# Kernel optimization log

Hardware: AMD Instinct MI355X
Metric: run time of the kernel (lower is better)

## Reference

```python
import jax, jax.numpy as jnp
import numpy as np

B, T, D = 2, 1024, 2048      # batch, seq_len, hidden_size
H, DK = 8, 128               # num_heads, head_k_dim
DV = 2 * DK                  # head_v_dim = head_dim * expand_v
KD, VD = H * DK, H * DV      # key_dim, value_dim
KCONV = 4                    # short conv kernel size
EPS = 1e-5


def _short_conv(x, w):
    # depthwise causal conv1d + SiLU; x: [B,T,C], w: [C,K]
    Klen = w.shape[1]
    xp = jnp.pad(x, ((0, 0), (Klen - 1, 0), (0, 0)))
    win = jnp.stack([xp[:, j:j + x.shape[1], :] for j in range(Klen)], axis=-1)  # [B,T,C,K]
    return jax.nn.silu(jnp.einsum('btck,ck->btc', win, w))


def _l2norm(x):
    return x * jax.lax.rsqrt(jnp.sum(x * x, -1, keepdims=True) + 1e-6)


def reference(hidden_states, q_w, k_w, v_w, a_w, b_w, g_w, o_w,
              q_conv_w, k_conv_w, v_conv_w, A_log, dt_bias, o_norm_w):
    h = hidden_states
    # projections + short depthwise causal conv + SiLU
    q = _short_conv(h @ q_w.T, q_conv_w)        # [B,T,KD]
    k = _short_conv(h @ k_w.T, k_conv_w)        # [B,T,KD]
    v = _short_conv(h @ v_w.T, v_conv_w)        # [B,T,VD]
    q = _l2norm(q.reshape(B, T, H, DK))
    k = _l2norm(k.reshape(B, T, H, DK))
    v = v.reshape(B, T, H, DV)
    beta = jax.nn.sigmoid(h @ b_w.T)                                 # [B,T,H]
    g = -jnp.exp(A_log) * jax.nn.softplus(h @ a_w.T + dt_bias)       # [B,T,H] decay log-gate
    scale = DK ** -0.5

    def step(S, xs):
        # S: [B,H,DK,DV] recurrent state; gated delta rule update
        qt, kt, vt, gt, bt = xs
        S = S * jnp.exp(gt)[..., None, None]
        kv = jnp.einsum('bhk,bhkv->bhv', kt, S)
        u = (vt - kv) * bt[..., None]
        S = S + jnp.einsum('bhk,bhv->bhkv', kt, u)
        ot = jnp.einsum('bhk,bhkv->bhv', qt, S) * scale
        return S, ot

    xs = (q.transpose(1, 0, 2, 3), k.transpose(1, 0, 2, 3), v.transpose(1, 0, 2, 3),
          g.transpose(1, 0, 2), beta.transpose(1, 0, 2))
    S0 = jnp.zeros((B, H, DK, DV), q.dtype)
    _, o = jax.lax.scan(step, S0, xs)
    o = o.transpose(1, 0, 2, 3)                       # [B,T,H,DV]
    # gated RMSNorm (FusedRMSNormGated) + output projection
    gate = (h @ g_w.T).reshape(B, T, H, DV)
    o = o * jax.lax.rsqrt(jnp.mean(o * o, -1, keepdims=True) + EPS) * o_norm_w
    o = o * jax.nn.silu(gate)
    return o.reshape(B, T, VD) @ o_w.T


def setup_inputs() -> dict:
    key = jax.random.key(0)
    ks = jax.random.split(key, 14)
    n = lambda i, shp, sc: jax.random.normal(ks[i], shp, jnp.float32) * sc
    return {
        'hidden_states': n(0, (B, T, D), 1.0),
        'q_w': n(1, (KD, D), 0.02), 'k_w': n(2, (KD, D), 0.02), 'v_w': n(3, (VD, D), 0.02),
        'a_w': n(4, (H, D), 0.02), 'b_w': n(5, (H, D), 0.02),
        'g_w': n(6, (VD, D), 0.02), 'o_w': n(7, (D, VD), 0.02),
        'q_conv_w': n(8, (KD, KCONV), 0.3), 'k_conv_w': n(9, (KD, KCONV), 0.3),
        'v_conv_w': n(10, (VD, KCONV), 0.3),
        'A_log': jnp.log(jax.random.uniform(ks[11], (H,), jnp.float32, 0.5, 16.0)),
        'dt_bias': n(12, (H,), 1.0),
        'o_norm_w': jnp.ones((DV,), jnp.float32),
    }
```

## Files before the change

kernel.cpp:

```cpp
#include <hip/hip_runtime.h>
#include <cstdint>

#define T_LEN 1024
#define NBIG  6400
#define SCALE_Q 0.08838834764831843f

typedef __bf16 bf16;
typedef __bf16 bf16x8 __attribute__((ext_vector_type(8)));
typedef float  f32x4  __attribute__((ext_vector_type(4)));

__device__ __forceinline__ unsigned short f2bf(float f) {
  unsigned int u = __builtin_bit_cast(unsigned int, f);
  u += 0x7FFFu + ((u >> 16) & 1u);
  return (unsigned short)(u >> 16);
}
__device__ __forceinline__ float bf2f(unsigned short u) {
  return __builtin_bit_cast(float, (unsigned int)u << 16);
}
__device__ __forceinline__ float silu_f(float x) { return x / (1.f + __expf(-x)); }

#define GLDS(src, dst) \
  __builtin_amdgcn_global_load_lds( \
      (__attribute__((address_space(1))) void*)(void*)(src), \
      (__attribute__((address_space(3))) void*)(void*)(dst), 16, 0, 0)

__global__ __launch_bounds__(256) void prep_all(
    const float* __restrict__ h,
    const float* __restrict__ qw, const float* __restrict__ kw,
    const float* __restrict__ vw, const float* __restrict__ gw,
    const float* __restrict__ aw, const float* __restrict__ bw,
    unsigned short* __restrict__ hbf, unsigned short* __restrict__ Wb) {
  const int blk = blockIdx.x;
  const int tid = threadIdx.x;
  if (blk < 4096) {
    const int idx = blk * 256 + tid;
    float4 f = ((const float4*)h)[idx];
    ushort4 o = { f2bf(f.x), f2bf(f.y), f2bf(f.z), f2bf(f.w) };
    ((ushort4*)hbf)[idx] = o;
  } else {
    const int idx = (blk - 4096) * 256 + tid;
    const int r = idx >> 9;
    const int c = (idx & 511) << 2;
    const float* src;
    if      (r < 1024) src = qw + (size_t)r * 2048;
    else if (r < 2048) src = kw + (size_t)(r - 1024) * 2048;
    else if (r < 4096) src = vw + (size_t)(r - 2048) * 2048;
    else if (r < 6144) src = gw + (size_t)(r - 4096) * 2048;
    else if (r < 6152) src = aw + (size_t)(r - 6144) * 2048;
    else if (r < 6160) src = bw + (size_t)(r - 6152) * 2048;
    else               src = nullptr;
    ushort4 o;
    if (src) {
      float4 f = *(const float4*)(src + c);
      o = { f2bf(f.x), f2bf(f.y), f2bf(f.z), f2bf(f.w) };
    } else {
      o = { 0, 0, 0, 0 };
    }
    *(ushort4*)(Wb + (size_t)r * 2048 + c) = o;
  }
}

template <int BN, int WN, int T, bool BF16OUT, bool ATOMIC, int ILOG>
__global__ __launch_bounds__(T, 4) void gemm_pipe(
    const bf16* __restrict__ A, const bf16* __restrict__ Bm,
    void* __restrict__ Cv, int N, int K, int ldk) {
  constexpr int AI = (128 * 32) / (T * 8);
  constexpr int BI = (BN * 32) / (T * 8);
  constexpr int LOADS = AI + BI;
  __shared__ bf16 LA[3][128 * 32];
  __shared__ bf16 LB[3][BN * 32];
  const int tid = threadIdx.x;
  const int lane = tid & 63;
  const int wid = tid >> 6;
  const int wm = wid / WN, wn = wid % WN;
  const int bidAll = blockIdx.x;
  const int bid = ATOMIC ? (bidAll & ((1 << ILOG) - 1)) : bidAll;
  const long kofs = ATOMIC ? (long)(bidAll >> ILOG) * K : 0;
  const int xcd = bid & 7, jj = bid >> 3;
  const long brow = (long)(xcd + 8 * (jj & 1)) * 128;
  const long bcol = (long)(jj >> 1) * BN;

  f32x4 acc[4][4];
#pragma unroll
  for (int m = 0; m < 4; ++m)
#pragma unroll
    for (int n = 0; n < 4; ++n)
#pragma unroll
      for (int r = 0; r < 4; ++r) acc[m][n][r] = 0.f;

  const bf16* AgS[AI];
  const bf16* BgS[BI];
  int adst[AI], bdst[BI];
#pragma unroll
  for (int e = 0; e < AI; ++e) {
    const int flat = e * T + tid;
    const int row = flat >> 2;
    const int sl = (flat & 3) ^ ((row >> 1) & 3);
    AgS[e] = A + (brow + row) * (long)ldk + kofs + sl * 8;
    adst[e] = flat * 8;
  }
#pragma unroll
  for (int e = 0; e < BI; ++e) {
    const int flat = e * T + tid;
    const int row = flat >> 2;
    const int sl = (flat & 3) ^ ((row >> 1) & 3);
    BgS[e] = Bm + (bcol + row) * (long)ldk + kofs + sl * 8;
    bdst[e] = flat * 8;
  }

#define STAGE(kt, sb)                                              \
  {                                                                \
    const long ko = (long)(kt) * 32;                               \
    _Pragma("unroll")                                              \
    for (int e = 0; e < AI; ++e) GLDS(AgS[e] + ko, &LA[sb][0] + adst[e]); \
    _Pragma("unroll")                                              \
    for (int e = 0; e < BI; ++e) GLDS(BgS[e] + ko, &LB[sb][0] + bdst[e]); \
  }
#define WAIT_VM()                                                  \
  if constexpr (LOADS == 3) asm volatile("s_waitcnt vmcnt(3)" ::: "memory"); \
  else                      asm volatile("s_waitcnt vmcnt(4)" ::: "memory");

  const int r16 = lane & 15;
  const int ks = lane >> 4;
  const int pso = (ks ^ ((r16 >> 1) & 3)) * 8;
  int rdA[4], rdB[4];
#pragma unroll
  for (int i = 0; i < 4; ++i) rdA[i] = (wm * 64 + i * 16 + r16) * 32 + pso;
#pragma unroll
  for (int j = 0; j < 4; ++j) rdB[j] = (wn * 64 + j * 16 + r16) * 32 + pso;

  const int nkt = K >> 5;
  STAGE(0, 0);
  STAGE(1, 1);
  WAIT_VM();
  __builtin_amdgcn_s_barrier();

  bf16x8 af[4], bfr[4];
#pragma unroll
  for (int i = 0; i < 4; ++i) af[i] = *(const bf16x8*)(&LA[0][0] + rdA[i]);
#pragma unroll
  for (int j = 0; j < 4; ++j) bfr[j] = *(const bf16x8*)(&LB[0][0] + rdB[j]);

  for (int kt = 0; kt < nkt; ++kt) {
    const int kts = (kt + 2 < nkt) ? kt + 2 : nkt - 1;
    const int sb = (kt + 2) % 3;
    const int nb = (kt + 1) % 3;

    STAGE(kts, sb);
    __builtin_amdgcn_s_setprio(1);
#pragma unroll
    for (int i = 0; i < 4; ++i)
#pragma unroll
      for (int j = 0; j < 4; ++j)
        acc[i][j] = __builtin_amdgcn_mfma_f32_16x16x32_bf16(af[i], bfr[j], acc[i][j], 0, 0, 0);
    __builtin_amdgcn_s_setprio(0);

    asm volatile("s_waitcnt lgkmcnt(0)" ::: "memory");
    WAIT_VM();
    __builtin_amdgcn_s_barrier();
#pragma unroll
    for (int i = 0; i < 4; ++i) af[i] = *(const bf16x8*)(&LA[nb][0] + rdA[i]);
#pragma unroll
    for (int j = 0; j < 4; ++j) bfr[j] = *(const bf16x8*)(&LB[nb][0] + rdB[j]);
  }
#undef STAGE
#undef WAIT_VM

  const long row0 = brow + wm * 64 + ((lane >> 4) * 4);
  const long col0 = bcol + wn * 64 + (lane & 15);
#pragma unroll
  for (int m = 0; m < 4; ++m)
#pragma unroll
    for (int n = 0; n < 4; ++n)
#pragma unroll
      for (int r = 0; r < 4; ++r) {
        const long idx = (row0 + m * 16 + r) * (long)N + col0 + n * 16;
        if constexpr (ATOMIC)
          atomicAdd((float*)Cv + idx, acc[m][n][r]);
        else if constexpr (BF16OUT)
          ((unsigned short*)Cv)[idx] = f2bf(acc[m][n][r]);
        else
          ((float*)Cv)[idx] = acc[m][n][r];
      }
}

template <int M, int N, int K, int NW>
__device__ __forceinline__ void mm_nt_lds(const unsigned short* A, const unsigned short* B,
                                          unsigned short* outG, int ldg, int tid) {
  constexpr int NT16 = N / 16;
  constexpr int PW = (M / 16) * NT16 / NW;
  const int w = tid >> 6, l = tid & 63;
  const int row = l & 15, ko = (l >> 4) * 8;
  f32x4 acc[PW];
#pragma unroll
  for (int i = 0; i < PW; ++i)
#pragma unroll
    for (int r = 0; r < 4; ++r) acc[i][r] = 0.f;
#pragma unroll
  for (int i = 0; i < PW; ++i) {
    const int ti = w + NW * i;
    const int rt = ti / NT16, ct = ti % NT16;
#pragma unroll
    for (int kk = 0; kk < K / 32; ++kk) {
      bf16x8 af = *(const bf16x8*)(A + (rt * 16 + row) * K + kk * 32 + ko);
      bf16x8 bf = *(const bf16x8*)(B + (ct * 16 + row) * K + kk * 32 + ko);
      acc[i] = __builtin_amdgcn_mfma_f32_16x16x32_bf16(af, bf, acc[i], 0, 0, 0);
    }
  }
#pragma unroll
  for (int i = 0; i < PW; ++i) {
    const int ti = w + NW * i;
    const int rt = ti / NT16, ct = ti % NT16;
    const int r0 = rt * 16 + (l >> 4) * 4;
    const int col = ct * 16 + (l & 15);
#pragma unroll
    for (int r = 0; r < 4; ++r)
      outG[(size_t)(r0 + r) * ldg + col] = f2bf(acc[i][r]);
  }
}

template <int K>
__device__ __forceinline__ void mm64_acc(const unsigned short* A, const unsigned short* B,
                                         f32x4 acc[2], int w, int row, int ko) {
#pragma unroll
  for (int i = 0; i < 2; ++i) {
    const int ti = w + 8 * i;
    const int rt = ti >> 2, ct = ti & 3;
#pragma unroll
    for (int kk = 0; kk < K / 32; ++kk) {
      bf16x8 af = *(const bf16x8*)(A + (rt * 16 + row) * K + kk * 32 + ko);
      bf16x8 bf = *(const bf16x8*)(B + (ct * 16 + row) * K + kk * 32 + ko);
      acc[i] = __builtin_amdgcn_mfma_f32_16x16x32_bf16(af, bf, acc[i], 0, 0, 0);
    }
  }
}

__global__ __launch_bounds__(512, 4) void chunk_prep(
    const unsigned short* __restrict__ Y,
    const float* __restrict__ qcw, const float* __restrict__ kcw, const float* __restrict__ vcw,
    const float* __restrict__ A_log, const float* __restrict__ dt_bias,
    unsigned short* __restrict__ Wg, unsigned short* __restrict__ Ubg,
    unsigned short* __restrict__ Attg, unsigned short* __restrict__ Qgg,
    unsigned short* __restrict__ KgTg, float* __restrict__ decg,
    const float* __restrict__ ow, unsigned short* __restrict__ owb,
    float* __restrict__ zout) {
  __shared__ unsigned short SM[36864];
  unsigned short* Kb_s   = SM;
  unsigned short* Qb_s   = SM + 8192;
  unsigned short* Xrow_s = SM + 16384;
  unsigned short* Mb_s   = SM + 20480;
  unsigned short* Xt_s   = SM + 24576;
  unsigned short* Yt_s   = SM + 28672;
  unsigned short* VbT_s  = SM + 20480;
  __shared__ float carr_s[64];
  __shared__ float beta_s[64];

  const int tid = threadIdx.x;
  const int ch = blockIdx.x;
  if (ch >= 256) {
    const int i = ch - 256;
    if (i < 512) {
#pragma unroll
      for (int e = 0; e < 4; ++e) {
        const int idx = e * 262144 + i * 512 + tid;
        float4 f = ((const float4*)ow)[idx];
        ushort4 o = { f2bf(f.x), f2bf(f.y), f2bf(f.z), f2bf(f.w) };
        ((ushort4*)owb)[idx] = o;
      }
    } else {
      const int i2 = i - 512;
      float4 z = {0.f, 0.f, 0.f, 0.f};
#pragma unroll
      for (int e = 0; e < 4; ++e) {
        const int idx = e * 262144 + i2 * 512 + tid;
        ((float4*)zout)[idx] = z;
      }
    }
    return;
  }

  const int w = tid >> 6, l = tid & 63;
  const int row16 = l & 15, ko = (l >> 4) * 8;
  const int bh = ch >> 4, p = ch & 15;
  const int b = bh >> 3, h = bh & 7;
  const size_t tbase = (size_t)b * T_LEN + p * 64;
  const bool head = (p == 0);

  if (tid < 64) {
    const unsigned short* Yr = Y + (tbase + tid) * NBIG;
    float a = bf2f(Yr[6144 + h]) + dt_bias[h];
    float sp = (a > 20.f) ? a : log1pf(expf(a));
    float g = -expf(A_log[h]) * sp;
    float bp = bf2f(Yr[6152 + h]);
    beta_s[tid] = 1.f / (1.f + expf(-bp));
    float c = g;
#pragma unroll
    for (int d = 1; d < 64; d <<= 1) {
      float y = __shfl_up(c, d);
      if (tid >= d) c += y;
    }
    carr_s[tid] = c;
    if (tid == 63) decg[ch] = __expf(c);
  }
  __syncthreads();

  {
    const bool isQ = (tid < 256);
    const int wk = tid & 255;
    const int quad = wk & 31, tg = wk >> 5;
    const int c = quad * 4;
    const float* cw = isQ ? qcw : kcw;
    const int cb = (isQ ? 0 : 1024) + h * 128 + c;
    float4 wv[4];
#pragma unroll
    for (int e = 0; e < 4; ++e) wv[e] = ((const float4*)cw)[h * 128 + c + e];
    float rows[11][4];
#pragma unroll
    for (int r = 0; r < 11; ++r) {
      if (head && tg == 0 && r < 3) {
        rows[r][0] = rows[r][1] = rows[r][2] = rows[r][3] = 0.f;
      } else {
        const ushort4 x = *(const ushort4*)(Y + (tbase + tg * 8 - 3 + r) * NBIG + cb);
        rows[r][0] = bf2f(x.x); rows[r][1] = bf2f(x.y);
        rows[r][2] = bf2f(x.z); rows[r][3] = bf2f(x.w);
      }
    }
    unsigned short* dst = isQ ? Qb_s : Kb_s;
    const float sc = isQ ? SCALE_Q : 1.f;
#pragma unroll
    for (int i = 0; i < 8; ++i) {
      float acc[4], ss = 0.f;
#pragma unroll
      for (int e = 0; e < 4; ++e) {
        float a = wv[e].x * rows[i][e];
        a = fmaf(wv[e].y, rows[i + 1][e], a);
        a = fmaf(wv[e].z, rows[i + 2][e], a);
        a = fmaf(wv[e].w, rows[i + 3][e], a);
        a = silu_f(a);
        acc[e] = a;
        ss += a * a;
      }
#pragma unroll
      for (int m = 16; m >= 1; m >>= 1) ss += __shfl_xor(ss, m);
      const float rn = rsqrtf(ss + 1e-6f) * sc;
      ushort4 o = {f2bf(acc[0] * rn), f2bf(acc[1] * rn), f2bf(acc[2] * rn), f2bf(acc[3] * rn)};
      *(ushort4*)(dst + (tg * 8 + i) * 128 + c) = o;
    }
  }
  __syncthreads();

  float xf[2][4];
  {
    f32x4 acc[2];
#pragma unroll
    for (int i = 0; i < 2; ++i)
#pragma unroll
      for (int r = 0; r < 4; ++r) acc[i][r] = 0.f;
    mm64_acc<128>(Kb_s, Kb_s, acc, w, row16, ko);
#pragma unroll
    for (int i = 0; i < 2; ++i) {
      const int ti = w + 8 * i;
      const int rt = ti >> 2, ct = ti & 3;
      const int r0 = rt * 16 + (l >> 4) * 4;
      const int col = ct * 16 + (l & 15);
#pragma unroll
      for (int r = 0; r < 4; ++r) {
        const int t = r0 + r, j = col;
        const float av = (j < t) ? beta_s[t] * __expf(carr_s[t] - carr_s[j]) * acc[i][r] : 0.f;
        const float dg = (t == j) ? 1.f : 0.f;
        Mb_s[t * 64 + j] = f2bf(dg + av);
        const float x0 = dg - av;
        xf[i][r] = x0;
        const unsigned short xb = f2bf(x0);
        Xrow_s[t * 64 + j] = xb;
        Xt_s[j * 64 + t] = xb;
      }
    }
  }
  __syncthreads();
  for (int it = 0; it < 5; ++it) {
    {
      f32x4 acc[2];
#pragma unroll
      for (int i = 0; i < 2; ++i)
#pragma unroll
        for (int r = 0; r < 4; ++r) acc[i][r] = 0.f;
      mm64_acc<64>(Mb_s, Xt_s, acc, w, row16, ko);
#pragma unroll
      for (int i = 0; i < 2; ++i) {
        const int ti = w + 8 * i;
        const int rt = ti >> 2, ct = ti & 3;
        const int r0 = rt * 16 + (l >> 4) * 4;
        const int col = ct * 16 + (l & 15);
#pragma unroll
        for (int r = 0; r < 4; ++r)
          Yt_s[col * 64 + (r0 + r)] = f2bf(acc[i][r]);
      }
    }
    __syncthreads();
    {
      f32x4 acc[2];
#pragma unroll
      for (int i = 0; i < 2; ++i)
#pragma unroll
        for (int r = 0; r < 4; ++r) acc[i][r] = 0.f;
      mm64_acc<64>(Xrow_s, Yt_s, acc, w, row16, ko);
      __syncthreads();
#pragma unroll
      for (int i = 0; i < 2; ++i) {
        const int ti = w + 8 * i;
        const int rt = ti >> 2, ct = ti & 3;
        const int r0 = rt * 16 + (l >> 4) * 4;
        const int col = ct * 16 + (l & 15);
#pragma unroll
        for (int r = 0; r < 4; ++r) {
          const float xn = 2.f * xf[i][r] - acc[i][r];
          xf[i][r] = xn;
          const unsigned short xb = f2bf(xn);
          Xrow_s[(r0 + r) * 64 + col] = xb;
          Xt_s[col * 64 + (r0 + r)] = xb;
        }
      }
    }
    __syncthreads();
  }
  const float ctot = carr_s[63];
  {
    const int quad = tid & 63, tg = tid >> 6;
    const int c = quad * 4;
    float4 wv[4];
#pragma unroll
    for (int e = 0; e < 4; ++e) wv[e] = ((const float4*)vcw)[h * 256 + c + e];
    float rows[11][4];
#pragma unroll
    for (int r = 0; r < 11; ++r) {
      if (head && tg == 0 && r < 3) {
        rows[r][0] = rows[r][1] = rows[r][2] = rows[r][3] = 0.f;
      } else {
        const ushort4 x = *(const ushort4*)(Y + (tbase + tg * 8 - 3 + r) * NBIG + 2048 + h * 256 + c);
        rows[r][0] = bf2f(x.x); rows[r][1] = bf2f(x.y);
        rows[r][2] = bf2f(x.z); rows[r][3] = bf2f(x.w);
      }
    }
#pragma unroll
    for (int i = 0; i < 8; ++i) {
      const int t = tg * 8 + i;
      const float bt = beta_s[t];
#pragma unroll
      for (int e = 0; e < 4; ++e) {
        float a = wv[e].x * rows[i][e];
        a = fmaf(wv[e].y, rows[i + 1][e], a);
        a = fmaf(wv[e].z, rows[i + 2][e], a);
        a = fmaf(wv[e].w, rows[i + 3][e], a);
        VbT_s[(c + e) * 64 + t] = f2bf(bt * silu_f(a));
      }
    }
  }
  {
    f32x4 acc[2];
#pragma unroll
    for (int i = 0; i < 2; ++i)
#pragma unroll
      for (int r = 0; r < 4; ++r) acc[i][r] = 0.f;
    mm64_acc<128>(Qb_s, Kb_s, acc, w, row16, ko);
#pragma unroll
    for (int i = 0; i < 2; ++i) {
      const int ti = w + 8 * i;
      const int rt = ti >> 2, ct = ti & 3;
      const int r0 = rt * 16 + (l >> 4) * 4;
      const int col = ct * 16 + (l & 15);
#pragma unroll
      for (int r = 0; r < 4; ++r) {
        const int t = r0 + r, j = col;
        const float av = (j <= t) ? __expf(carr_s[t] - carr_s[j]) * acc[i][r] : 0.f;
        Attg[(size_t)ch * 4096 + t * 64 + j] = f2bf(av);
      }
    }
  }
#pragma unroll
  for (int i = 0; i < 16; ++i) {
    const int idx = i * 512 + tid;
    const int t = idx >> 7;
    Qgg[(size_t)ch * 8192 + idx] = f2bf(__expf(carr_s[t]) * bf2f(Qb_s[idx]));
  }
#pragma unroll
  for (int i = 0; i < 16; ++i) {
    const int idx = i * 512 + tid;
    const int d = idx >> 6, t = idx & 63;
    KgTg[(size_t)ch * 8192 + idx] = f2bf(__expf(ctot - carr_s[t]) * bf2f(Kb_s[t * 128 + d]));
  }
  __syncthreads();
  unsigned short* KbgT = Qb_s;
#pragma unroll
  for (int i = 0; i < 16; ++i) {
    const int idx = i * 512 + tid;
    const int d = idx >> 6, t = idx & 63;
    KbgT[idx] = f2bf(beta_s[t] * __expf(carr_s[t]) * bf2f(Kb_s[t * 128 + d]));
  }
  __syncthreads();
  mm_nt_lds<64, 128, 64, 8>(Xrow_s, KbgT, Wg + (size_t)ch * 8192, 128, tid);
  mm_nt_lds<64, 256, 64, 8>(Xrow_s, VbT_s, Ubg + (size_t)ch * 16384, 256, tid);
}

__device__ __forceinline__ void p2_stage(
    const unsigned short* Wg, const unsigned short* Attg, const unsigned short* Qgg,
    const unsigned short* KgTg, const unsigned short* Ubg,
    int ch, int vb, unsigned short* buf, int tid) {
#pragma unroll
  for (int i = 0; i < 2; ++i) {
    const int f = i * 512 + tid;
    GLDS(Wg + (size_t)ch * 8192 + f * 8, (char*)buf + f * 16);
  }
  {
    const int f = tid;
    GLDS(Attg + (size_t)ch * 4096 + f * 8, (char*)(buf + 8192) + f * 16);
  }
#pragma unroll
  for (int i = 0; i < 2; ++i) {
    const int f = i * 512 + tid;
    GLDS(Qgg + (size_t)ch * 8192 + f * 8, (char*)(buf + 12288) + f * 16);
  }
#pragma unroll
  for (int i = 0; i < 2; ++i) {
    const int f = i * 512 + tid;
    GLDS(KgTg + (size_t)ch * 8192 + f * 8, (char*)(buf + 20480) + f * 16);
  }
  if (tid < 128) {
    const int f = tid;
    const int t = f >> 1, c8 = f & 1;
    GLDS(Ubg + (size_t)ch * 16384 + t * 256 + vb * 16 + c8 * 8, (char*)(buf + 28672) + f * 16);
  }
}

__global__ __launch_bounds__(512, 1) void scan_chunks(
    const unsigned short* __restrict__ Wg, const unsigned short* __restrict__ Ubg,
    const unsigned short* __restrict__ Attg, const unsigned short* __restrict__ Qgg,
    const unsigned short* __restrict__ KgTg, const float* __restrict__ decg,
    float* __restrict__ osc) {
  __shared__ float StT_s[16 * 128];
  __shared__ unsigned short StTb_s[16 * 128];
  __shared__ unsigned short uT_s[16 * 64];
  __shared__ unsigned short stage_s[2][29696];

  const int tid = threadIdx.x;
  const int w = tid >> 6, l = tid & 63;
  const int row = l & 15, ko = (l >> 4) * 8;
  const int blk = blockIdx.x;
  const int vb = blk >> 4, bh = blk & 15;
  const int b = bh >> 3, h = bh & 7;
  const bool uw = (w < 4);

  for (int i = tid; i < 2048; i += 512) { StT_s[i] = 0.f; StTb_s[i] = 0; }
  p2_stage(Wg, Attg, Qgg, KgTg, Ubg, bh * 16, vb, stage_s[0], tid);

  for (int p = 0; p < 16; ++p) {
    unsigned short* bufc = stage_s[p & 1];
    const unsigned short* Wl   = bufc;
    const unsigned short* Attl = bufc + 8192;
    const unsigned short* Qgl  = bufc + 12288;
    const unsigned short* KgTl = bufc + 20480;
    const unsigned short* Ubl  = bufc + 28672;
    __syncthreads();

    f32x4 uacc;
#pragma unroll
    for (int r = 0; r < 4; ++r) uacc[r] = 0.f;
    if (uw) {
#pragma unroll
      for (int kk = 0; kk < 4; ++kk) {
        bf16x8 af = *(const bf16x8*)(Wl + (w * 16 + row) * 128 + kk * 32 + ko);
        bf16x8 bf = *(const bf16x8*)(StTb_s + row * 128 + kk * 32 + ko);
        uacc = __builtin_amdgcn_mfma_f32_16x16x32_bf16(af, bf, uacc, 0, 0, 0);
      }
      const int r0 = w * 16 + (l >> 4) * 4;
      const int col = l & 15;
#pragma unroll
      for (int r = 0; r < 4; ++r) {
        const int t = r0 + r;
        const float ubv = bf2f(Ubl[t * 16 + col]);
        uT_s[col * 64 + t] = f2bf(ubv - uacc[r]);
      }
    }
    __syncthreads();
    if (p < 15)
      p2_stage(Wg, Attg, Qgg, KgTg, Ubg, bh * 16 + p + 1, vb, stage_s[(p + 1) & 1], tid);

    f32x4 oacc;
#pragma unroll
    for (int r = 0; r < 4; ++r) oacc[r] = 0.f;
    if (uw) {
#pragma unroll
      for (int kk = 0; kk < 4; ++kk) {
        bf16x8 af = *(const bf16x8*)(Qgl + (w * 16 + row) * 128 + kk * 32 + ko);
        bf16x8 bf = *(const bf16x8*)(StTb_s + row * 128 + kk * 32 + ko);
        oacc = __builtin_amdgcn_mfma_f32_16x16x32_bf16(af, bf, oacc, 0, 0, 0);
      }
#pragma unroll
      for (int kk = 0; kk < 2; ++kk) {
        bf16x8 af = *(const bf16x8*)(Attl + (w * 16 + row) * 64 + kk * 32 + ko);
        bf16x8 bf = *(const bf16x8*)(uT_s + row * 64 + kk * 32 + ko);
        oacc = __builtin_amdgcn_mfma_f32_16x16x32_bf16(af, bf, oacc, 0, 0, 0);
      }
    }
    f32x4 sacc;
#pragma unroll
    for (int r = 0; r < 4; ++r) sacc[r] = 0.f;
#pragma unroll
    for (int kk = 0; kk < 2; ++kk) {
      bf16x8 af = *(const bf16x8*)(uT_s + row * 64 + kk * 32 + ko);
      bf16x8 bf = *(const bf16x8*)(KgTl + (w * 16 + row) * 64 + kk * 32 + ko);
      sacc = __builtin_amdgcn_mfma_f32_16x16x32_bf16(af, bf, sacc, 0, 0, 0);
    }
    const float dec = decg[bh * 16 + p];
    __syncthreads();

    if (uw) {
      const int r0 = w * 16 + (l >> 4) * 4;
      const int col = l & 15;
#pragma unroll
      for (int r = 0; r < 4; ++r) {
        const size_t trow = (size_t)b * T_LEN + p * 64 + r0 + r;
        osc[(trow * 8 + h) * 256 + vb * 16 + col] = oacc[r];
      }
    }
    {
      const int cold = w * 16 + (l & 15);
#pragma unroll
      for (int r = 0; r < 4; ++r) {
        const int idx = ((l >> 4) * 4 + r) * 128 + cold;
        const float sn = fmaf(dec, StT_s[idx], sacc[r]);
        StT_s[idx] = sn;
        StTb_s[idx] = f2bf(sn);
      }
    }
  }
}

__global__ __launch_bounds__(256) void rmsgate(
    const float* __restrict__ ob, const unsigned short* __restrict__ Y,
    const float* __restrict__ onw, unsigned short* __restrict__ Obf) {
  const int bt = blockIdx.x;
  const int tid = threadIdx.x;
  const int c = tid * 8;
  const float* orow = ob + (size_t)bt * 2048 + c;
  const unsigned short* grow = Y + (size_t)bt * NBIG + 4096 + c;
  const float4 o0 = *(const float4*)orow, o1 = *(const float4*)(orow + 4);
  const ushort4 g0 = *(const ushort4*)grow, g1 = *(const ushort4*)(grow + 4);
  const float ov[8] = {o0.x, o0.y, o0.z, o0.w, o1.x, o1.y, o1.z, o1.w};
  const float gv[8] = {bf2f(g0.x), bf2f(g0.y), bf2f(g0.z), bf2f(g0.w),
                       bf2f(g1.x), bf2f(g1.y), bf2f(g1.z), bf2f(g1.w)};
  float ss = 0.f;
#pragma unroll
  for (int e = 0; e < 8; ++e) ss += ov[e] * ov[e];
#pragma unroll
  for (int m = 16; m >= 1; m >>= 1) ss += __shfl_xor(ss, m);
  const float rn = rsqrtf(ss * (1.f / 256.f) + 1e-5f);
  const int dv = c & 255;
  unsigned short rr[8];
#pragma unroll
  for (int e = 0; e < 8; ++e) {
    const float val = ov[e] * rn * onw[dv + e] * silu_f(gv[e]);
    rr[e] = f2bf(val);
  }
  ushort4 r0 = {rr[0], rr[1], rr[2], rr[3]};
  ushort4 r1 = {rr[4], rr[5], rr[6], rr[7]};
  *(ushort4*)(Obf + (size_t)bt * 2048 + c) = r0;
  *(ushort4*)(Obf + (size_t)bt * 2048 + c + 4) = r1;
}

extern "C" void kernel_launch(void* const* d_in, const int* in_sizes, int n_in,
                              void* d_out, int out_size, void* d_ws, size_t ws_size,
                              hipStream_t stream) {
  (void)in_sizes; (void)n_in; (void)out_size; (void)ws_size;
  const float* h    = (const float*)d_in[0];
  const float* qw   = (const float*)d_in[1];
  const float* kw   = (const float*)d_in[2];
  const float* vw   = (const float*)d_in[3];
  const float* aw   = (const float*)d_in[4];
  const float* bw   = (const float*)d_in[5];
  const float* gw   = (const float*)d_in[6];
  const float* ow   = (const float*)d_in[7];
  const float* qcw  = (const float*)d_in[8];
  const float* kcw  = (const float*)d_in[9];
  const float* vcw  = (const float*)d_in[10];
  const float* Alog = (const float*)d_in[11];
  const float* dtb  = (const float*)d_in[12];
  const float* onw  = (const float*)d_in[13];

  char* ws = (char*)d_ws;
  size_t off = 0;
  auto alloc = [&](size_t bytes) {
    char* p = ws + off;
    off = (off + bytes + 255) & ~(size_t)255;
    return p;
  };
  unsigned short* hbf  = (unsigned short*)alloc(2048ull * 2048 * 2);
  unsigned short* Wb   = (unsigned short*)alloc((size_t)NBIG * 2048 * 2);
  unsigned short* owb  = (unsigned short*)alloc(2048ull * 2048 * 2);
  unsigned short* Ybf  = (unsigned short*)alloc(2048ull * NBIG * 2);
  float* osc           = (float*)alloc(2048ull * 2048 * 4);
  unsigned short* Obf  = (unsigned short*)alloc(2048ull * 2048 * 2);
  unsigned short* Wg   = (unsigned short*)alloc(256ull * 8192 * 2);
  unsigned short* Ubg  = (unsigned short*)alloc(256ull * 16384 * 2);
  unsigned short* Attg = (unsigned short*)alloc(256ull * 4096 * 2);
  unsigned short* Qgg  = (unsigned short*)alloc(256ull * 8192 * 2);
  unsigned short* KgTg = (unsigned short*)alloc(256ull * 8192 * 2);
  float* decg          = (float*)alloc(256ull * 4);

  prep_all<<<16896, 256, 0, stream>>>(h, qw, kw, vw, gw, aw, bw, hbf, Wb);
  gemm_pipe<256, 4, 512, true, false, 0><<<400, 512, 0, stream>>>(
      (const bf16*)hbf, (const bf16*)Wb, Ybf, NBIG, 2048, 2048);
  chunk_prep<<<1280, 512, 0, stream>>>(Ybf, qcw, kcw, vcw, Alog, dtb,
                                       Wg, Ubg, Attg, Qgg, KgTg, decg,
                                       ow, owb, (float*)d_out);
  scan_chunks<<<256, 512, 0, stream>>>(Wg, Ubg, Attg, Qgg, KgTg, decg, osc);
  rmsgate<<<2048, 256, 0, stream>>>(osc, Ybf, onw, Obf);
  gemm_pipe<256, 4, 512, false, true, 7><<<256, 512, 0, stream>>>(
      (const bf16*)Obf, (const bf16*)owb, d_out, 2048, 1024, 2048);
}
```

Measured before the change: 208.9 us.

## Load scan chunk operands straight into registers instead of double-buffered LDS staging

The chunk scan kernel no longer stages W, Att, Qg, KgT and U tiles through a double-buffered LDS region with global_load_lds prefetch. Each wave now loads its MFMA fragments for the current chunk straight from global memory into registers at the top of each iteration. The state fragments and uT fragments are reused across the MFMAs, and one barrier per iteration is dropped. This removes LDS round trips and the large shared allocation, but the global load latency is no longer hidden behind the previous chunk's compute, because nothing is prefetched ahead.

New measurement: 207.3 us. Within noise of the previous version (-0.7%).

```diff
diff --git a/kernel.cpp b/kernel.cpp
--- a/kernel.cpp
+++ b/kernel.cpp
@@ -502,36 +502,6 @@
   mm_nt_lds<64, 256, 64, 8>(Xrow_s, VbT_s, Ubg + (size_t)ch * 16384, 256, tid);
 }
 
-__device__ __forceinline__ void p2_stage(
-    const unsigned short* Wg, const unsigned short* Attg, const unsigned short* Qgg,
-    const unsigned short* KgTg, const unsigned short* Ubg,
-    int ch, int vb, unsigned short* buf, int tid) {
-#pragma unroll
-  for (int i = 0; i < 2; ++i) {
-    const int f = i * 512 + tid;
-    GLDS(Wg + (size_t)ch * 8192 + f * 8, (char*)buf + f * 16);
-  }
-  {
-    const int f = tid;
-    GLDS(Attg + (size_t)ch * 4096 + f * 8, (char*)(buf + 8192) + f * 16);
-  }
-#pragma unroll
-  for (int i = 0; i < 2; ++i) {
-    const int f = i * 512 + tid;
-    GLDS(Qgg + (size_t)ch * 8192 + f * 8, (char*)(buf + 12288) + f * 16);
-  }
-#pragma unroll
-  for (int i = 0; i < 2; ++i) {
-    const int f = i * 512 + tid;
-    GLDS(KgTg + (size_t)ch * 8192 + f * 8, (char*)(buf + 20480) + f * 16);
-  }
-  if (tid < 128) {
-    const int f = tid;
-    const int t = f >> 1, c8 = f & 1;
-    GLDS(Ubg + (size_t)ch * 16384 + t * 256 + vb * 16 + c8 * 8, (char*)(buf + 28672) + f * 16);
-  }
-}
-
 __global__ __launch_bounds__(512, 1) void scan_chunks(
     const unsigned short* __restrict__ Wg, const unsigned short* __restrict__ Ubg,
     const unsigned short* __restrict__ Attg, const unsigned short* __restrict__ Qgg,
@@ -540,7 +510,6 @@
   __shared__ float StT_s[16 * 128];
   __shared__ unsigned short StTb_s[16 * 128];
   __shared__ unsigned short uT_s[16 * 64];
-  __shared__ unsigned short stage_s[2][29696];
 
   const int tid = threadIdx.x;
   const int w = tid >> 6, l = tid & 63;
@@ -549,74 +518,75 @@
   const int vb = blk >> 4, bh = blk & 15;
   const int b = bh >> 3, h = bh & 7;
   const bool uw = (w < 4);
+  const int r0 = w * 16 + (l >> 4) * 4;
+  const int col = l & 15;
 
   for (int i = tid; i < 2048; i += 512) { StT_s[i] = 0.f; StTb_s[i] = 0; }
-  p2_stage(Wg, Attg, Qgg, KgTg, Ubg, bh * 16, vb, stage_s[0], tid);
 
   for (int p = 0; p < 16; ++p) {
-    unsigned short* bufc = stage_s[p & 1];
-    const unsigned short* Wl   = bufc;
-    const unsigned short* Attl = bufc + 8192;
-    const unsigned short* Qgl  = bufc + 12288;
-    const unsigned short* KgTl = bufc + 20480;
-    const unsigned short* Ubl  = bufc + 28672;
+    const size_t ch = (size_t)(bh * 16 + p);
+    const unsigned short* Wp   = Wg   + ch * 8192;
+    const unsigned short* Attp = Attg + ch * 4096;
+    const unsigned short* Qgp  = Qgg  + ch * 8192;
+    const unsigned short* KgTp = KgTg + ch * 8192;
+    const unsigned short* Ubp  = Ubg  + ch * 16384;
+    const float dec = decg[ch];
+
+    bf16x8 wf[4], qf[4], atf[2], kf[2];
+    float ubv[4];
+    if (uw) {
+#pragma unroll
+      for (int kk = 0; kk < 4; ++kk) wf[kk]  = *(const bf16x8*)(Wp  + (w * 16 + row) * 128 + kk * 32 + ko);
+#pragma unroll
+      for (int kk = 0; kk < 4; ++kk) qf[kk]  = *(const bf16x8*)(Qgp + (w * 16 + row) * 128 + kk * 32 + ko);
+#pragma unroll
+      for (int kk = 0; kk < 2; ++kk) atf[kk] = *(const bf16x8*)(Attp + (w * 16 + row) * 64 + kk * 32 + ko);
+#pragma unroll
+      for (int r = 0; r < 4; ++r)    ubv[r]  = bf2f(Ubp[(r0 + r) * 256 + vb * 16 + col]);
+    }
+#pragma unroll
+    for (int kk = 0; kk < 2; ++kk)   kf[kk]  = *(const bf16x8*)(KgTp + (w * 16 + row) * 64 + kk * 32 + ko);
+
     __syncthreads();
 
+    bf16x8 stf[4];
     f32x4 uacc;
 #pragma unroll
     for (int r = 0; r < 4; ++r) uacc[r] = 0.f;
     if (uw) {
 #pragma unroll
       for (int kk = 0; kk < 4; ++kk) {
-        bf16x8 af = *(const bf16x8*)(Wl + (w * 16 + row) * 128 + kk * 32 + ko);
-        bf16x8 bf = *(const bf16x8*)(StTb_s + row * 128 + kk * 32 + ko);
-        uacc = __builtin_amdgcn_mfma_f32_16x16x32_bf16(af, bf, uacc, 0, 0, 0);
-      }
-      const int r0 = w * 16 + (l >> 4) * 4;
-      const int col = l & 15;
-#pragma unroll
-      for (int r = 0; r < 4; ++r) {
-        const int t = r0 + r;
-        const float ubv = bf2f(Ubl[t * 16 + col]);
-        uT_s[col * 64 + t] = f2bf(ubv - uacc[r]);
-      }
+        stf[kk] = *(const bf16x8*)(StTb_s + row * 128 + kk * 32 + ko);
+        uacc = __builtin_amdgcn_mfma_f32_16x16x32_bf16(wf[kk], stf[kk], uacc, 0, 0, 0);
+      }
+#pragma unroll
+      for (int r = 0; r < 4; ++r)
+        uT_s[col * 64 + (r0 + r)] = f2bf(ubv[r] - uacc[r]);
     }
     __syncthreads();
-    if (p < 15)
-      p2_stage(Wg, Attg, Qgg, KgTg, Ubg, bh * 16 + p + 1, vb, stage_s[(p + 1) & 1], tid);
 
     f32x4 oacc;
 #pragma unroll
     for (int r = 0; r < 4; ++r) oacc[r] = 0.f;
+    bf16x8 utf[2];
+#pragma unroll
+    for (int kk = 0; kk < 2; ++kk) utf[kk] = *(const bf16x8*)(uT_s + row * 64 + kk * 32 + ko);
     if (uw) {
 #pragma unroll
-      for (int kk = 0; kk < 4; ++kk) {
-        bf16x8 af = *(const bf16x8*)(Qgl + (w * 16 + row) * 128 + kk * 32 + ko);
-        bf16x8 bf = *(const bf16x8*)(StTb_s + row * 128 + kk * 32 + ko);
-        oacc = __builtin_amdgcn_mfma_f32_16x16x32_bf16(af, bf, oacc, 0, 0, 0);
-      }
-#pragma unroll
-      for (int kk = 0; kk < 2; ++kk) {
-        bf16x8 af = *(const bf16x8*)(Attl + (w * 16 + row) * 64 + kk * 32 + ko);
-        bf16x8 bf = *(const bf16x8*)(uT_s + row * 64 + kk * 32 + ko);
-        oacc = __builtin_amdgcn_mfma_f32_16x16x32_bf16(af, bf, oacc, 0, 0, 0);
-      }
+      for (int kk = 0; kk < 4; ++kk)
+        oacc = __builtin_amdgcn_mfma_f32_16x16x32_bf16(qf[kk], stf[kk], oacc, 0, 0, 0);
+#pragma unroll
+      for (int kk = 0; kk < 2; ++kk)
+        oacc = __builtin_amdgcn_mfma_f32_16x16x32_bf16(atf[kk], utf[kk], oacc, 0, 0, 0);
     }
     f32x4 sacc;
 #pragma unroll
     for (int r = 0; r < 4; ++r) sacc[r] = 0.f;
 #pragma unroll
-    for (int kk = 0; kk < 2; ++kk) {
-      bf16x8 af = *(const bf16x8*)(uT_s + row * 64 + kk * 32 + ko);
-      bf16x8 bf = *(const bf16x8*)(KgTl + (w * 16 + row) * 64 + kk * 32 + ko);
-      sacc = __builtin_amdgcn_mfma_f32_16x16x32_bf16(af, bf, sacc, 0, 0, 0);
-    }
-    const float dec = decg[bh * 16 + p];
-    __syncthreads();
+    for (int kk = 0; kk < 2; ++kk)
+      sacc = __builtin_amdgcn_mfma_f32_16x16x32_bf16(utf[kk], kf[kk], sacc, 0, 0, 0);
 
     if (uw) {
-      const int r0 = w * 16 + (l >> 4) * 4;
-      const int col = l & 15;
 #pragma unroll
       for (int r = 0; r < 4; ++r) {
         const size_t trow = (size_t)b * T_LEN + p * 64 + r0 + r;
```
